# Kernel optimization log

Measured on AMD Instinct MI355X. Metric: run time of the kernel, lower is better.

## Reference

```python
import jax, jax.numpy as jnp
import numpy as np

MIN_NORM = 1e-15
PROJ_EPS = 4e-3  # hgcn PoincareBall eps for float32
C = 1.0          # curvature (c_in == c_out == 1.0)


def artanh(x):
    x = jnp.clip(x, -1.0 + 1e-7, 1.0 - 1e-7)
    return 0.5 * (jnp.log1p(x) - jnp.log1p(-x))


def _norm(x):
    return jnp.maximum(jnp.linalg.norm(x, axis=-1, keepdims=True), MIN_NORM)


def proj(x, c):
    norm = _norm(x)
    maxnorm = (1.0 - PROJ_EPS) / jnp.sqrt(c)
    return jnp.where(norm > maxnorm, x / norm * maxnorm, x)


def expmap0(u, c):
    sc = jnp.sqrt(c)
    un = _norm(u)
    return jnp.tanh(sc * un) * u / (sc * un)


def logmap0(p, c):
    sc = jnp.sqrt(c)
    pn = _norm(p)
    return artanh(sc * pn) * p / (sc * pn)


def mobius_add(x, y, c):
    x2 = jnp.sum(x * x, axis=-1, keepdims=True)
    y2 = jnp.sum(y * y, axis=-1, keepdims=True)
    xy = jnp.sum(x * y, axis=-1, keepdims=True)
    num = (1.0 + 2.0 * c * xy + c * y2) * x + (1.0 - c * x2) * y
    den = 1.0 + 2.0 * c * xy + c * c * x2 * y2
    return num / jnp.maximum(den, MIN_NORM)


def mobius_matvec(m, x, c):
    # m: [out, in], x: [N, in] on the Poincare ball
    sc = jnp.sqrt(c)
    xn = _norm(x)
    mx = x @ m.T                      # [N, out]
    mxn = _norm(mx)
    res = jnp.tanh(mxn / xn * artanh(sc * xn)) * mx / (mxn * sc)
    zero = jnp.all(mx == 0, axis=-1, keepdims=True)
    return jnp.where(zero, jnp.zeros_like(res), res)


def setup_inputs() -> dict:
    key = jax.random.key(0)
    ks = jax.random.split(key, 6)
    N, IN, OUT = 1546, 1546, 64
    # hyperbolic input features: expmap0 of a small tangent vector, then proj
    x_tan = jax.random.normal(ks[0], (N, IN), jnp.float32) * 0.01
    x = proj(expmap0(x_tan, C), C)
    adj = jax.random.uniform(ks[1], (N, N), jnp.float32)
    adj = adj / jnp.sum(adj, axis=1, keepdims=True)  # row-normalized adjacency
    xav = np.sqrt(2.0) * np.sqrt(2.0 / (IN + OUT))   # xavier_uniform std-ish scale
    W_drug = jax.random.normal(ks[2], (OUT, IN), jnp.float32) * xav
    W_micr = jax.random.normal(ks[3], (OUT, IN), jnp.float32) * xav
    bias_drug = jnp.zeros((OUT,), jnp.float32)
    bias_micr = jnp.zeros((OUT,), jnp.float32)
    wn_scale = np.sqrt(2.0) * np.sqrt(2.0 / (128 + 64))
    weightnode = jax.random.normal(ks[4], (128, 64), jnp.float32) * wn_scale
    biasnode = jnp.zeros((N, 1), jnp.float32)
    return {"x": x, "adj": adj, "W_drug": W_drug, "W_micr": W_micr,
            "bias_drug": bias_drug, "bias_micr": bias_micr,
            "weightnode": weightnode, "biasnode": biasnode}


def _hyp_linear(x, W, bias, c):
    mv = proj(mobius_matvec(W, x, c), c)
    hyp_bias = proj(expmap0(bias[None, :], c), c)  # proj_tan0 is identity on Poincare
    return proj(mobius_add(mv, hyp_bias, c), c)


def reference(x, adj, W_drug, W_micr, bias_drug, bias_micr, weightnode, biasnode):
    N_DRUG, N_MICR = 1373, 173
    # ---- HypLinear (x.shape[1] == 1546 branch) ----
    res_drug = _hyp_linear(x, W_drug, bias_drug, C)
    res_micr = _hyp_linear(x, W_micr, bias_micr, C)
    liner_h = jnp.concatenate([res_drug[:N_DRUG], res_micr[-N_MICR:]], axis=0)  # [1546, 64]
    # ---- HypAgg (use_att=False: spmm aggregation in tangent space at origin) ----
    x_tangent = logmap0(liner_h, C)          # [1546, 64]
    support_t = adj @ x_tangent              # [1546, 64]
    agg_h = proj(expmap0(support_t, C), C)
    # ---- HypAct (gated mix; the logmap0/expmap0 'result' is dead code, overwritten) ----
    zf = jnp.concatenate([agg_h, liner_h], axis=1)          # [1546, 128]
    delt1 = jax.nn.relu(zf @ weightnode + biasnode)         # [1546, 64]
    h = delt1 * agg_h + (1.0 - delt1) * liner_h
    return h, adj
```

## Files before the change

kernel.cpp:

```cpp
#include <hip/hip_runtime.h>
#include <math.h>

#define NROWS 1546
#define INDIM 1546
#define ODIM  64
#define NDRUG 1373
#define MINN  1e-15f
#define MAXNRM 0.996f

#define KSTEPS 49
#define FRAGSZ (KSTEPS * 4 * 512)
#define REDS   65

typedef short  short8 __attribute__((ext_vector_type(8)));
typedef float  f32x4  __attribute__((ext_vector_type(4)));

__device__ __forceinline__ unsigned short f2bf(float f) {
    unsigned u = __float_as_uint(f);
    u += 0x7FFFu + ((u >> 16) & 1u);
    return (unsigned short)(u >> 16);
}

__device__ __forceinline__ int fragaddr(int k, int col) {
    return ((k >> 5) * 4 + (col >> 4)) * 512 + (((k & 31) >> 3) * 16 + (col & 15)) * 8 + (k & 7);
}

__device__ __forceinline__ float artanh_(float x) {
    x = fminf(fmaxf(x, -1.0f + 1e-7f), 1.0f - 1e-7f);
    return 0.5f * (log1pf(x) - log1pf(-x));
}

__device__ __forceinline__ float wsum(float v) {
#pragma unroll
    for (int off = 32; off > 0; off >>= 1) v += __shfl_xor(v, off, 64);
    return v;
}

__global__ void prep_kernel(const float* __restrict__ Wd, const float* __restrict__ Wm,
                            unsigned short* __restrict__ WfD, unsigned short* __restrict__ WfM,
                            const float* __restrict__ bd, const float* __restrict__ bm,
                            float* __restrict__ hbD, float* __restrict__ hbM,
                            float* __restrict__ hb2,
                            const float4* __restrict__ adj4, float4* __restrict__ adjout4,
                            int n4) {
    int tid = threadIdx.x;
    if (blockIdx.x < 64) {
        int total = 64 * 1568;
        for (int i = blockIdx.x * 256 + tid; i < total; i += 64 * 256) {
            int o = i / 1568, k = i - o * 1568;
            int addr = fragaddr(k, o);
            float vd = (k < INDIM) ? Wd[o * INDIM + k] : 0.f;
            float vm = (k < INDIM) ? Wm[o * INDIM + k] : 0.f;
            WfD[addr] = f2bf(vd);
            WfM[addr] = f2bf(vm);
        }
        return;
    }
    if (blockIdx.x == 64) {
        if (tid < 128) {
            int wave = tid >> 6, lane = tid & 63;
            const float* b = wave ? bm : bd;
            float v = b[lane];
            float un2 = wsum(v * v);
            float un = fmaxf(sqrtf(un2), MINN);
            float e = tanhf(un) * v / un;
            float en2 = wsum(e * e);
            float en = fmaxf(sqrtf(en2), MINN);
            float scl = (en > MAXNRM) ? (MAXNRM / en) : 1.0f;
            float* hb = wave ? hbM : hbD;
            hb[lane] = e * scl;
            if (lane == 0) hb2[wave] = en2 * scl * scl;
        }
        return;
    }
    int nb = gridDim.x - 65;
    for (int i = (blockIdx.x - 65) * 256 + tid; i < n4; i += nb * 256)
        adjout4[i] = adj4[i];
}

__global__ __launch_bounds__(512) void liner_fused(
    const float* __restrict__ X,
    const unsigned short* __restrict__ WfD, const unsigned short* __restrict__ WfM,
    const float* __restrict__ hbD, const float* __restrict__ hbM, const float* __restrict__ hb2v,
    float* __restrict__ liner, unsigned short* __restrict__ xtf) {
    __shared__ float red[8][16][REDS];
    __shared__ float ssl[8][16];
    int tid = threadIdx.x, kc = tid >> 6, lane = tid & 63;
    int lrow = lane & 15, lgrp = lane >> 4;
    int s = blockIdx.x;
    int strip = (s == 97) ? 85 : s;
    int rowbase = strip * 16;
    const unsigned short* Bf = (s <= 85) ? WfD : WfM;
    int lo = (s == 97) ? NDRUG : 0;
    int hi = (s == 85) ? NDRUG : NROWS;
    const float* arow = X + (size_t)min(rowbase + lrow, NROWS - 1) * INDIM;

    f32x4 ac0 = {0,0,0,0}, ac1 = {0,0,0,0}, ac2 = {0,0,0,0}, ac3 = {0,0,0,0};
    float ss = 0.f;
    for (int ks = kc; ks < 48; ks += 8) {
        const float* xp = arow + ks * 32 + lgrp * 8;
        float2 p0 = *(const float2*)(xp);
        float2 p1 = *(const float2*)(xp + 2);
        float2 p2 = *(const float2*)(xp + 4);
        float2 p3 = *(const float2*)(xp + 6);
        float xv[8] = {p0.x, p0.y, p1.x, p1.y, p2.x, p2.y, p3.x, p3.y};
        short8 av;
#pragma unroll
        for (int j = 0; j < 8; ++j) { ss = fmaf(xv[j], xv[j], ss); av[j] = (short)f2bf(xv[j]); }
        const unsigned short* bp = Bf + (size_t)(ks * 4) * 512 + lane * 8;
        short8 b0 = *(const short8*)(bp);
        short8 b1 = *(const short8*)(bp + 512);
        short8 b2 = *(const short8*)(bp + 1024);
        short8 b3 = *(const short8*)(bp + 1536);
        ac0 = __builtin_amdgcn_mfma_f32_16x16x32_bf16(av, b0, ac0, 0, 0, 0);
        ac1 = __builtin_amdgcn_mfma_f32_16x16x32_bf16(av, b1, ac1, 0, 0, 0);
        ac2 = __builtin_amdgcn_mfma_f32_16x16x32_bf16(av, b2, ac2, 0, 0, 0);
        ac3 = __builtin_amdgcn_mfma_f32_16x16x32_bf16(av, b3, ac3, 0, 0, 0);
    }
    if (kc == 0) {
        short8 av;
#pragma unroll
        for (int j = 0; j < 8; ++j) {
            int k = 1536 + lgrp * 8 + j;
            float v = (k < INDIM) ? arow[k] : 0.f;
            ss = fmaf(v, v, ss);
            av[j] = (short)f2bf(v);
        }
        const unsigned short* bp = Bf + (size_t)(48 * 4) * 512 + lane * 8;
        short8 b0 = *(const short8*)(bp);
        short8 b1 = *(const short8*)(bp + 512);
        short8 b2 = *(const short8*)(bp + 1024);
        short8 b3 = *(const short8*)(bp + 1536);
        ac0 = __builtin_amdgcn_mfma_f32_16x16x32_bf16(av, b0, ac0, 0, 0, 0);
        ac1 = __builtin_amdgcn_mfma_f32_16x16x32_bf16(av, b1, ac1, 0, 0, 0);
        ac2 = __builtin_amdgcn_mfma_f32_16x16x32_bf16(av, b2, ac2, 0, 0, 0);
        ac3 = __builtin_amdgcn_mfma_f32_16x16x32_bf16(av, b3, ac3, 0, 0, 0);
    }
    ss += __shfl_xor(ss, 16, 64);
    ss += __shfl_xor(ss, 32, 64);
    if (lane < 16) ssl[kc][lrow] = ss;
#pragma unroll
    for (int i = 0; i < 4; ++i) {
        int r = lgrp * 4 + i;
        red[kc][r][lrow]      = ac0[i];
        red[kc][r][16 + lrow] = ac1[i];
        red[kc][r][32 + lrow] = ac2[i];
        red[kc][r][48 + lrow] = ac3[i];
    }
    __syncthreads();

#pragma unroll
    for (int j = 0; j < 2; ++j) {
        int r = 2 * kc + j;
        int grow = rowbase + r;
        if (grow >= lo && grow < hi) {
            float mx = 0.f, xn2 = 0.f;
#pragma unroll
            for (int w = 0; w < 8; ++w) { mx += red[w][r][lane]; xn2 += ssl[w][r]; }
            float mxn2 = wsum(mx * mx);
            float xn = fmaxf(sqrtf(xn2), MINN);
            float mxn = fmaxf(sqrtf(mxn2), MINN);
            float g = mxn / xn * artanh_(xn);
            float t = tanhf(g);
            float res = t * mx / mxn;
            float rn = fabsf(t);
            if (rn > MAXNRM) { res *= MAXNRM / rn; rn = MAXNRM; }
            const float* hb = (grow < NDRUG) ? hbD : hbM;
            float y = hb[lane];
            float y2 = hb2v[(grow < NDRUG) ? 0 : 1];
            float x2 = rn * rn;
            float xy = wsum(res * y);
            float num = (1.0f + 2.0f * xy + y2) * res + (1.0f - x2) * y;
            float den = 1.0f + 2.0f * xy + x2 * y2;
            float v = num / fmaxf(den, MINN);
            float v2 = wsum(v * v);
            float vn = fmaxf(sqrtf(v2), MINN);
            if (vn > MAXNRM) { v *= MAXNRM / vn; vn = MAXNRM; }
            float xt = artanh_(vn) / vn * v;
            liner[(size_t)grow * ODIM + lane] = v;
            xtf[fragaddr(grow, lane)] = f2bf(xt);
        }
    }
    if (s == 96) {
        for (int row = NROWS + kc; row < 1568; row += 8)
            xtf[fragaddr(row, lane)] = 0;
    }
}

__global__ __launch_bounds__(512) void agg_fused(
    const float* __restrict__ ADJ, const unsigned short* __restrict__ xtf,
    const float* __restrict__ liner, const float* __restrict__ WN ,
    const float* __restrict__ biasnode, float* __restrict__ out_h) {
    __shared__ float red[8][16][REDS];
    __shared__ float zl[16][128];
    int tid = threadIdx.x, kc = tid >> 6, lane = tid & 63;
    int lrow = lane & 15, lgrp = lane >> 4;
    int rowbase = blockIdx.x * 16;
    const float* arow = ADJ + (size_t)min(rowbase + lrow, NROWS - 1) * INDIM;

    f32x4 ac0 = {0,0,0,0}, ac1 = {0,0,0,0}, ac2 = {0,0,0,0}, ac3 = {0,0,0,0};
    for (int ks = kc; ks < 48; ks += 8) {
        const float* xp = arow + ks * 32 + lgrp * 8;
        float2 p0 = *(const float2*)(xp);
        float2 p1 = *(const float2*)(xp + 2);
        float2 p2 = *(const float2*)(xp + 4);
        float2 p3 = *(const float2*)(xp + 6);
        float xv[8] = {p0.x, p0.y, p1.x, p1.y, p2.x, p2.y, p3.x, p3.y};
        short8 av;
#pragma unroll
        for (int j = 0; j < 8; ++j) av[j] = (short)f2bf(xv[j]);
        const unsigned short* bp = xtf + (size_t)(ks * 4) * 512 + lane * 8;
        short8 b0 = *(const short8*)(bp);
        short8 b1 = *(const short8*)(bp + 512);
        short8 b2 = *(const short8*)(bp + 1024);
        short8 b3 = *(const short8*)(bp + 1536);
        ac0 = __builtin_amdgcn_mfma_f32_16x16x32_bf16(av, b0, ac0, 0, 0, 0);
        ac1 = __builtin_amdgcn_mfma_f32_16x16x32_bf16(av, b1, ac1, 0, 0, 0);
        ac2 = __builtin_amdgcn_mfma_f32_16x16x32_bf16(av, b2, ac2, 0, 0, 0);
        ac3 = __builtin_amdgcn_mfma_f32_16x16x32_bf16(av, b3, ac3, 0, 0, 0);
    }
    if (kc == 0) {
        short8 av;
#pragma unroll
        for (int j = 0; j < 8; ++j) {
            int k = 1536 + lgrp * 8 + j;
            av[j] = (short)f2bf((k < INDIM) ? arow[k] : 0.f);
        }
        const unsigned short* bp = xtf + (size_t)(48 * 4) * 512 + lane * 8;
        short8 b0 = *(const short8*)(bp);
        short8 b1 = *(const short8*)(bp + 512);
        short8 b2 = *(const short8*)(bp + 1024);
        short8 b3 = *(const short8*)(bp + 1536);
        ac0 = __builtin_amdgcn_mfma_f32_16x16x32_bf16(av, b0, ac0, 0, 0, 0);
        ac1 = __builtin_amdgcn_mfma_f32_16x16x32_bf16(av, b1, ac1, 0, 0, 0);
        ac2 = __builtin_amdgcn_mfma_f32_16x16x32_bf16(av, b2, ac2, 0, 0, 0);
        ac3 = __builtin_amdgcn_mfma_f32_16x16x32_bf16(av, b3, ac3, 0, 0, 0);
    }
#pragma unroll
    for (int i = 0; i < 4; ++i) {
        int r = lgrp * 4 + i;
        red[kc][r][lrow]      = ac0[i];
        red[kc][r][16 + lrow] = ac1[i];
        red[kc][r][32 + lrow] = ac2[i];
        red[kc][r][48 + lrow] = ac3[i];
    }
    __syncthreads();

#pragma unroll
    for (int j = 0; j < 2; ++j) {
        int r = 2 * kc + j;
        int grow = rowbase + r;
        if (grow < NROWS) {
            float sv = 0.f;
#pragma unroll
            for (int w = 0; w < 8; ++w) sv += red[w][r][lane];
            float sn2 = wsum(sv * sv);
            float sn = fmaxf(sqrtf(sn2), MINN);
            float th = tanhf(sn);
            float agg = th * sv / sn;
            if (th > MAXNRM) agg *= MAXNRM / th;
            float lin = liner[(size_t)grow * ODIM + lane];
            zl[r][lane] = agg;
            zl[r][64 + lane] = lin;
            float d = biasnode[grow];
            const float* w = WN + lane;
#pragma unroll 8
            for (int f = 0; f < 128; ++f) d = fmaf(zl[r][f], w[f * 64], d);
            d = fmaxf(d, 0.0f);
            out_h[(size_t)grow * ODIM + lane] = d * agg + (1.0f - d) * lin;
        }
    }
}

extern "C" void kernel_launch(void* const* d_in, const int* in_sizes, int n_in,
                              void* d_out, int out_size, void* d_ws, size_t ws_size,
                              hipStream_t stream) {
    const float* x   = (const float*)d_in[0];
    const float* adj = (const float*)d_in[1];
    const float* Wd  = (const float*)d_in[2];
    const float* Wm  = (const float*)d_in[3];
    const float* bd  = (const float*)d_in[4];
    const float* bm  = (const float*)d_in[5];
    const float* wn  = (const float*)d_in[6];
    const float* bn  = (const float*)d_in[7];
    float* out = (float*)d_out;

    const int WELEMS = ODIM * INDIM;
    unsigned short* WfD = (unsigned short*)d_ws;
    unsigned short* WfM = WfD + FRAGSZ;
    unsigned short* xtf = WfM + FRAGSZ;
    float* hbD   = (float*)(xtf + FRAGSZ);
    float* hbM   = hbD + 64;
    float* hb2   = hbM + 64;
    float* liner = hbD + 192;

    int n4 = (NROWS * NROWS) / 4;
    prep_kernel<<<512, 256, 0, stream>>>(Wd, Wm, WfD, WfM, bd, bm, hbD, hbM, hb2,
                                         (const float4*)adj, (float4*)(out + WELEMS), n4);
    liner_fused<<<98, 512, 0, stream>>>(x, WfD, WfM, hbD, hbM, hb2, liner, xtf);
    agg_fused<<<97, 512, 0, stream>>>(adj, xtf, liner, wn, bn, out);
}
```

Measured before the change: 35.59 us.

## Move adj passthrough copy into aggregation kernel and precompute row norms separately

The passthrough copy of adj to the output moves out of the prep kernel, which shrinks from 512 to 65 blocks, and into agg_fused. There each block copies its own 16 rows of adj before running the MFMA loop, so those rows should be in cache when the loop reads them again. In liner_fused, the per-row squared norm of X is now computed up front by a direct row pass instead of inside the MFMA loop, which drops the shared-memory ssl reduction. The main k-loops are also fully unrolled. The trade-off is that the copy is now spread over only 97 blocks and serialized ahead of the aggregation math, and X rows are read twice in liner_fused.

```diff
diff --git a/kernel.cpp b/kernel.cpp
--- a/kernel.cpp
+++ b/kernel.cpp
@@ -40,9 +40,7 @@
                             unsigned short* __restrict__ WfD, unsigned short* __restrict__ WfM,
                             const float* __restrict__ bd, const float* __restrict__ bm,
                             float* __restrict__ hbD, float* __restrict__ hbM,
-                            float* __restrict__ hb2,
-                            const float4* __restrict__ adj4, float4* __restrict__ adjout4,
-                            int n4) {
+                            float* __restrict__ hb2) {
     int tid = threadIdx.x;
     if (blockIdx.x < 64) {
         int total = 64 * 1568;
@@ -56,26 +54,20 @@
         }
         return;
     }
-    if (blockIdx.x == 64) {
-        if (tid < 128) {
-            int wave = tid >> 6, lane = tid & 63;
-            const float* b = wave ? bm : bd;
-            float v = b[lane];
-            float un2 = wsum(v * v);
-            float un = fmaxf(sqrtf(un2), MINN);
-            float e = tanhf(un) * v / un;
-            float en2 = wsum(e * e);
-            float en = fmaxf(sqrtf(en2), MINN);
-            float scl = (en > MAXNRM) ? (MAXNRM / en) : 1.0f;
-            float* hb = wave ? hbM : hbD;
-            hb[lane] = e * scl;
-            if (lane == 0) hb2[wave] = en2 * scl * scl;
-        }
-        return;
-    }
-    int nb = gridDim.x - 65;
-    for (int i = (blockIdx.x - 65) * 256 + tid; i < n4; i += nb * 256)
-        adjout4[i] = adj4[i];
+    if (tid < 128) {
+        int wave = tid >> 6, lane = tid & 63;
+        const float* b = wave ? bm : bd;
+        float v = b[lane];
+        float un2 = wsum(v * v);
+        float un = fmaxf(sqrtf(un2), MINN);
+        float e = tanhf(un) * v / un;
+        float en2 = wsum(e * e);
+        float en = fmaxf(sqrtf(en2), MINN);
+        float scl = (en > MAXNRM) ? (MAXNRM / en) : 1.0f;
+        float* hb = wave ? hbM : hbD;
+        hb[lane] = e * scl;
+        if (lane == 0) hb2[wave] = en2 * scl * scl;
+    }
 }
 
 __global__ __launch_bounds__(512) void liner_fused(
@@ -84,7 +76,6 @@
     const float* __restrict__ hbD, const float* __restrict__ hbM, const float* __restrict__ hb2v,
     float* __restrict__ liner, unsigned short* __restrict__ xtf) {
     __shared__ float red[8][16][REDS];
-    __shared__ float ssl[8][16];
     int tid = threadIdx.x, kc = tid >> 6, lane = tid & 63;
     int lrow = lane & 15, lgrp = lane >> 4;
     int s = blockIdx.x;
@@ -93,11 +84,25 @@
     const unsigned short* Bf = (s <= 85) ? WfD : WfM;
     int lo = (s == 97) ? NDRUG : 0;
     int hi = (s == 85) ? NDRUG : NROWS;
+
+    float xn2r[2];
+#pragma unroll
+    for (int j = 0; j < 2; ++j) {
+        int gr = min(rowbase + 2 * kc + j, NROWS - 1);
+        const float2* src = (const float2*)(X + (size_t)gr * INDIM);
+        float ss = 0.f;
+        for (int c = lane; c < 773; c += 64) {
+            float2 v = src[c];
+            ss = fmaf(v.x, v.x, fmaf(v.y, v.y, ss));
+        }
+        xn2r[j] = wsum(ss);
+    }
+
     const float* arow = X + (size_t)min(rowbase + lrow, NROWS - 1) * INDIM;
-
     f32x4 ac0 = {0,0,0,0}, ac1 = {0,0,0,0}, ac2 = {0,0,0,0}, ac3 = {0,0,0,0};
-    float ss = 0.f;
-    for (int ks = kc; ks < 48; ks += 8) {
+#pragma unroll
+    for (int ii = 0; ii < 6; ++ii) {
+        int ks = kc + 8 * ii;
         const float* xp = arow + ks * 32 + lgrp * 8;
         float2 p0 = *(const float2*)(xp);
         float2 p1 = *(const float2*)(xp + 2);
@@ -106,7 +111,7 @@
         float xv[8] = {p0.x, p0.y, p1.x, p1.y, p2.x, p2.y, p3.x, p3.y};
         short8 av;
 #pragma unroll
-        for (int j = 0; j < 8; ++j) { ss = fmaf(xv[j], xv[j], ss); av[j] = (short)f2bf(xv[j]); }
+        for (int j = 0; j < 8; ++j) av[j] = (short)f2bf(xv[j]);
         const unsigned short* bp = Bf + (size_t)(ks * 4) * 512 + lane * 8;
         short8 b0 = *(const short8*)(bp);
         short8 b1 = *(const short8*)(bp + 512);
@@ -122,9 +127,7 @@
 #pragma unroll
         for (int j = 0; j < 8; ++j) {
             int k = 1536 + lgrp * 8 + j;
-            float v = (k < INDIM) ? arow[k] : 0.f;
-            ss = fmaf(v, v, ss);
-            av[j] = (short)f2bf(v);
+            av[j] = (short)f2bf((k < INDIM) ? arow[k] : 0.f);
         }
         const unsigned short* bp = Bf + (size_t)(48 * 4) * 512 + lane * 8;
         short8 b0 = *(const short8*)(bp);
@@ -136,9 +139,6 @@
         ac2 = __builtin_amdgcn_mfma_f32_16x16x32_bf16(av, b2, ac2, 0, 0, 0);
         ac3 = __builtin_amdgcn_mfma_f32_16x16x32_bf16(av, b3, ac3, 0, 0, 0);
     }
-    ss += __shfl_xor(ss, 16, 64);
-    ss += __shfl_xor(ss, 32, 64);
-    if (lane < 16) ssl[kc][lrow] = ss;
 #pragma unroll
     for (int i = 0; i < 4; ++i) {
         int r = lgrp * 4 + i;
@@ -154,9 +154,10 @@
         int r = 2 * kc + j;
         int grow = rowbase + r;
         if (grow >= lo && grow < hi) {
-            float mx = 0.f, xn2 = 0.f;
-#pragma unroll
-            for (int w = 0; w < 8; ++w) { mx += red[w][r][lane]; xn2 += ssl[w][r]; }
+            float mx = 0.f;
+#pragma unroll
+            for (int w = 0; w < 8; ++w) mx += red[w][r][lane];
+            float xn2 = xn2r[j];
             float mxn2 = wsum(mx * mx);
             float xn = fmaxf(sqrtf(xn2), MINN);
             float mxn = fmaxf(sqrtf(mxn2), MINN);
@@ -190,16 +191,29 @@
 __global__ __launch_bounds__(512) void agg_fused(
     const float* __restrict__ ADJ, const unsigned short* __restrict__ xtf,
     const float* __restrict__ liner, const float* __restrict__ WN ,
-    const float* __restrict__ biasnode, float* __restrict__ out_h) {
+    const float* __restrict__ biasnode, float* __restrict__ out_h,
+    float* __restrict__ adj_out) {
     __shared__ float red[8][16][REDS];
     __shared__ float zl[16][128];
     int tid = threadIdx.x, kc = tid >> 6, lane = tid & 63;
     int lrow = lane & 15, lgrp = lane >> 4;
     int rowbase = blockIdx.x * 16;
+
+#pragma unroll
+    for (int j = 0; j < 2; ++j) {
+        int gr = rowbase + 2 * kc + j;
+        if (gr < NROWS) {
+            const float2* src = (const float2*)(ADJ + (size_t)gr * INDIM);
+            float2* dst = (float2*)(adj_out + (size_t)gr * INDIM);
+            for (int c = lane; c < 773; c += 64) dst[c] = src[c];
+        }
+    }
+
     const float* arow = ADJ + (size_t)min(rowbase + lrow, NROWS - 1) * INDIM;
-
     f32x4 ac0 = {0,0,0,0}, ac1 = {0,0,0,0}, ac2 = {0,0,0,0}, ac3 = {0,0,0,0};
-    for (int ks = kc; ks < 48; ks += 8) {
+#pragma unroll
+    for (int ii = 0; ii < 6; ++ii) {
+        int ks = kc + 8 * ii;
         const float* xp = arow + ks * 32 + lgrp * 8;
         float2 p0 = *(const float2*)(xp);
         float2 p1 = *(const float2*)(xp + 2);
@@ -294,9 +308,7 @@
     float* hb2   = hbM + 64;
     float* liner = hbD + 192;
 
-    int n4 = (NROWS * NROWS) / 4;
-    prep_kernel<<<512, 256, 0, stream>>>(Wd, Wm, WfD, WfM, bd, bm, hbD, hbM, hb2,
-                                         (const float4*)adj, (float4*)(out + WELEMS), n4);
+    prep_kernel<<<65, 256, 0, stream>>>(Wd, Wm, WfD, WfM, bd, bm, hbD, hbM, hb2);
     liner_fused<<<98, 512, 0, stream>>>(x, WfD, WfM, hbD, hbM, hb2, liner, xtf);
-    agg_fused<<<97, 512, 0, stream>>>(adj, xtf, liner, wn, bn, out);
-}
+    agg_fused<<<97, 512, 0, stream>>>(adj, xtf, liner, wn, bn, out, out + WELEMS);
+}
```

Result: slower. 46.48 us (+30.6%).
